# Kernel tuning notes

Hardware: AMD Instinct MI355X
Metric: run time of the kernel (lower is better)

Reference implementation:

```python
import jax, jax.numpy as jnp
import numpy as np

EMBED = 1024
HEADS = 16
HEAD_DIM = EMBED // HEADS
B, S = 2, 2048


def setup_inputs() -> dict:
    key = jax.random.key(0)
    ks = jax.random.split(key, 11)
    sc = 1.0 / np.sqrt(EMBED)
    return {
        "query": jax.random.normal(ks[0], (B, S, EMBED), jnp.float32),
        "key_in": jax.random.normal(ks[1], (B, S, EMBED), jnp.float32),
        "value": jax.random.normal(ks[2], (B, S, EMBED), jnp.float32),
        "Wq": jax.random.normal(ks[3], (EMBED, EMBED), jnp.float32) * sc,
        "bq": jnp.zeros((EMBED,), jnp.float32),
        "Wk": jax.random.normal(ks[4], (EMBED, EMBED), jnp.float32) * sc,
        "bk": jnp.zeros((EMBED,), jnp.float32),
        "Wv": jax.random.normal(ks[5], (EMBED, EMBED), jnp.float32) * sc,
        "bv": jnp.zeros((EMBED,), jnp.float32),
        "Wo": jax.random.normal(ks[6], (EMBED, EMBED), jnp.float32) * sc,
        "bo": jnp.zeros((EMBED,), jnp.float32),
    }


def reference(query, key_in, value, Wq, bq, Wk, bk, Wv, bv, Wo, bo):
    b = query.shape[0]
    # projections -> [B, H, S, Dh]
    def split_heads(x):
        return x.reshape(b, -1, HEADS, HEAD_DIM).transpose(0, 2, 1, 3)
    q = split_heads(query @ Wq + bq)
    k = split_heads(key_in @ Wk + bk)
    v = split_heads(value @ Wv + bv)
    scores = jnp.einsum("bhqd,bhkd->bhqk", q, k) / np.sqrt(HEAD_DIM).astype(jnp.float32)
    probs = jax.nn.softmax(scores, axis=-1)  # dropout in eval mode = identity
    ctx = jnp.einsum("bhqk,bhkd->bhqd", probs, v)
    ctx = ctx.transpose(0, 2, 1, 3).reshape(b, -1, EMBED)
    return ctx @ Wo + bo
```

## Files before the change

kernel.cpp:

```cpp
#include <hip/hip_runtime.h>

typedef unsigned short u16;
typedef unsigned int   u32;
typedef float   f32x4   __attribute__((ext_vector_type(4)));
typedef float   f32x16  __attribute__((ext_vector_type(16)));
typedef __bf16  bf16x8  __attribute__((ext_vector_type(8)));
typedef u16     u16x8   __attribute__((ext_vector_type(8)));
typedef u16     u16x4   __attribute__((ext_vector_type(4)));
typedef u32     u32x4   __attribute__((ext_vector_type(4)));

#define EMBED 1024
#define SEQ   2048
#define NH    16
#define HD    64

#define WS_WT  0u
#define WS_X   (8u<<20)
#define WS_QF  (32u<<20)
#define WS_CTX WS_X
#define WS_KF  (40u<<20)
#define WS_VF  (48u<<20)

__device__ __forceinline__ u16 f2bf(float f) {
  unsigned u = __builtin_bit_cast(unsigned, f);
  u += 0x7fffu + ((u >> 16) & 1u);
  return (u16)(u >> 16);
}

__device__ __forceinline__ u32 cvtpk(float lo, float hi) {
  u32 r;
  asm("v_cvt_pk_bf16_f32 %0, %1, %2" : "=v"(r) : "v"(lo), "v"(hi));
  return r;
}

__device__ __forceinline__ void gl16(const void* g, void* l) {
  __builtin_amdgcn_global_load_lds((__attribute__((address_space(1))) void*)g,
                                   (__attribute__((address_space(3))) void*)l,
                                   16, 0, 0);
}

__global__ __launch_bounds__(256) void cvt_kernel(const float* __restrict__ q,
                                                  const float* __restrict__ k,
                                                  const float* __restrict__ v,
                                                  u16* __restrict__ X) {
  const float* src = blockIdx.z == 0 ? q : blockIdx.z == 1 ? k : v;
  u16* dst = X + (size_t)blockIdx.z * 4194304u;
  size_t i = ((size_t)blockIdx.x * 256 + threadIdx.x) * 8;
  f32x4 a = *(const f32x4*)(src + i);
  f32x4 b = *(const f32x4*)(src + i + 4);
  u16x8 o;
#pragma unroll
  for (int j = 0; j < 4; ++j) { o[j] = f2bf(a[j]); o[4 + j] = f2bf(b[j]); }
  *(u16x8*)(dst + i) = o;
}

__global__ __launch_bounds__(256) void wtrans_kernel(const float* __restrict__ Wq,
                                                     const float* __restrict__ Wk,
                                                     const float* __restrict__ Wv,
                                                     const float* __restrict__ Wo,
                                                     u16* __restrict__ T) {
  const float* W = blockIdx.z == 0 ? Wq : blockIdx.z == 1 ? Wk : blockIdx.z == 2 ? Wv : Wo;
  u16* t = T + (size_t)blockIdx.z * 1048576u;
  __shared__ float sm[32][33];
  const int x = threadIdx.x, y = threadIdx.y;
  const int n0 = blockIdx.x * 32, k0 = blockIdx.y * 32;
#pragma unroll
  for (int i = 0; i < 4; ++i) sm[y + 8 * i][x] = W[(size_t)(k0 + y + 8 * i) * EMBED + n0 + x];
  __syncthreads();
#pragma unroll
  for (int i = 0; i < 4; ++i) t[(size_t)(n0 + y + 8 * i) * EMBED + k0 + x] = f2bf(sm[x][y + 8 * i]);
}

template <int MODE>
__global__ __launch_bounds__(256) void gemm128(char* __restrict__ ws,
                                               const float* __restrict__ bias0,
                                               const float* __restrict__ bias1,
                                               const float* __restrict__ bias2,
                                               float* __restrict__ out) {
  const int z = (MODE == 0) ? blockIdx.z : 0;
  const u16* A  = (MODE == 0) ? (const u16*)(ws + WS_X) + (size_t)z * 4194304u
                              : (const u16*)(ws + WS_CTX);
  const u16* Bt = (const u16*)(ws + WS_WT) + (size_t)((MODE == 0) ? z : 3) * 1048576u;
  const float* bias = (MODE == 0) ? (z == 0 ? bias0 : z == 1 ? bias1 : bias2) : bias0;

  __shared__ u16 lA[128 * 32];
  __shared__ u16 lB[128 * 32];

  const int tid = threadIdx.x, l = tid & 63, w = tid >> 6, g = l >> 4, li = l & 15;

  const int id = blockIdx.y * 8 + blockIdx.x;
  const int swz = (id & 7) * 32 + (id >> 3);
  const int m0 = (swz >> 3) * 128, n0 = (swz & 7) * 128;

  const int wr = (w >> 1) * 64, wc = (w & 1) * 64;
  const int schunk = l & 3;

  f32x4 acc[4][4] = {};

  for (int kt = 0; kt < 32; ++kt) {
    const int k0 = kt * 32;
#pragma unroll
    for (int c = 0; c < 2; ++c) {
      const int ci = w * 2 + c;
      const int row = ci * 16 + (l >> 2);
      const int kk = (schunk ^ (row & 3)) * 8;
      gl16(A + (size_t)(m0 + row) * 1024 + k0 + kk, &lA[ci * 512 + l * 8]);
    }
#pragma unroll
    for (int c = 0; c < 2; ++c) {
      const int ci = w * 2 + c;
      const int row = ci * 16 + (l >> 2);
      const int kk = (schunk ^ (row & 3)) * 8;
      gl16(Bt + (size_t)(n0 + row) * 1024 + k0 + kk, &lB[ci * 512 + l * 8]);
    }
    __syncthreads();

    bf16x8 af[4], bfr[4];
#pragma unroll
    for (int mf = 0; mf < 4; ++mf) {
      const int r = wr + mf * 16 + li;
      af[mf] = __builtin_bit_cast(bf16x8, *(const u16x8*)&lA[r * 32 + (g ^ (r & 3)) * 8]);
    }
#pragma unroll
    for (int nf = 0; nf < 4; ++nf) {
      const int r = wc + nf * 16 + li;
      bfr[nf] = __builtin_bit_cast(bf16x8, *(const u16x8*)&lB[r * 32 + (g ^ (r & 3)) * 8]);
    }
#pragma unroll
    for (int mf = 0; mf < 4; ++mf)
#pragma unroll
      for (int nf = 0; nf < 4; ++nf)
        acc[mf][nf] = __builtin_amdgcn_mfma_f32_16x16x32_bf16(af[mf], bfr[nf], acc[mf][nf], 0, 0, 0);
    __syncthreads();
  }

  u16* Qf = (u16*)(ws + WS_QF);
  u16* Kf = (u16*)(ws + WS_KF);
  u16* Vf = (u16*)(ws + WS_VF);
#pragma unroll
  for (int mf = 0; mf < 4; ++mf)
#pragma unroll
    for (int nf = 0; nf < 4; ++nf)
#pragma unroll
      for (int r4 = 0; r4 < 4; ++r4) {
        const int row = m0 + wr + mf * 16 + g * 4 + r4;
        const int col = n0 + wc + nf * 16 + li;
        float v = acc[mf][nf][r4] + bias[col];
        if (MODE == 1) {
          out[(size_t)row * 1024 + col] = v;
        } else {
          const int bb = row >> 11, s = row & 2047, hh = col >> 6, d = col & 63;
          const size_t fb = (size_t)(bb * 16 + hh) * 131072u;
          const size_t kfo = fb + (s >> 6) * 4096 + ((s >> 5) & 1) * 2048 + (d >> 4) * 512 +
                             ((d >> 3) & 1) * 256 + (s & 31) * 8 + (d & 7);
          if (z == 0) {
            Qf[kfo] = f2bf(v * 0.1803368801f);
          } else if (z == 1) {
            Kf[kfo] = f2bf(v);
          } else {
            const int k16 = s & 15;
            const int ks = (k16 & 3) | ((k16 & 4) << 1) | ((k16 & 8) >> 1);
            Vf[fb + (s >> 6) * 4096 + (d >> 5) * 2048 + ((s >> 5) & 1) * 1024 +
               ((s >> 4) & 1) * 512 + (ks >> 3) * 256 + (d & 31) * 8 + (ks & 7)] = f2bf(v);
          }
        }
      }
}

__global__ __launch_bounds__(64) void attn_kernel(char* __restrict__ ws) {
  const u16* QF = (const u16*)(ws + WS_QF);
  const u16* KF = (const u16*)(ws + WS_KF);
  const u16* VF = (const u16*)(ws + WS_VF);
  u16* ctx = (u16*)(ws + WS_CTX);

  const int l = threadIdx.x, l31 = l & 31, hi = l >> 5;

  const int id = blockIdx.y * 64 + blockIdx.x;
  const int sw = (id & 7) * 256 + (id >> 3);
  const int bh = sw >> 6, qt = sw & 63;

  const u16* Qp = QF + (size_t)bh * 131072u;
  const u16* Kp = KF + (size_t)bh * 131072u;
  const u16* Vp = VF + (size_t)bh * 131072u;
  const int q = qt * 32 + l31;

  bf16x8 qf[4];
#pragma unroll
  for (int kk = 0; kk < 4; ++kk)
    qf[kk] = __builtin_bit_cast(bf16x8, *(const u16x8*)(Qp + (qt * 4 + kk) * 512 + l * 8));

  f32x16 o0 = {}, o1 = {};
  float m = -1e30f, ls = 0.f;

  u16x8 ka[8], kb[8];
#pragma unroll
  for (int g = 0; g < 2; ++g)
#pragma unroll
    for (int kk = 0; kk < 4; ++kk)
      ka[g * 4 + kk] = *(const u16x8*)(Kp + (g * 4 + kk) * 512 + l * 8);

#define ATTN_BODY(KC, KN, T)                                                             \
  {                                                                                      \
    const int tn = ((T) + 1) & 31;                                                       \
    _Pragma("unroll")                                                                    \
    for (int g = 0; g < 2; ++g)                                                          \
      _Pragma("unroll")                                                                  \
      for (int kk = 0; kk < 4; ++kk)                                                     \
        KN[g * 4 + kk] = *(const u16x8*)(Kp + tn * 4096 + (g * 4 + kk) * 512 + l * 8);   \
    u16x8 vf[2][2][2];    \
    _Pragma("unroll")                                                                    \
    for (int g = 0; g < 2; ++g)                                                          \
      _Pragma("unroll")                                                                  \
      for (int dt = 0; dt < 2; ++dt)                                                     \
        _Pragma("unroll")                                                                \
        for (int kk = 0; kk < 2; ++kk)                                                   \
          vf[g][dt][kk] = *(const u16x8*)(Vp + (T) * 4096 +                              \
                                          (dt * 4 + g * 2 + kk) * 512 + l * 8);          \
    f32x16 s0 = {}, s1 = {};                                                             \
    __builtin_amdgcn_s_setprio(1);                                                       \
    _Pragma("unroll")                                                                    \
    for (int kk = 0; kk < 4; ++kk)                                                       \
      s0 = __builtin_amdgcn_mfma_f32_32x32x16_bf16(                                      \
          __builtin_bit_cast(bf16x8, KC[kk]), qf[kk], s0, 0, 0, 0);                      \
    _Pragma("unroll")                                                                    \
    for (int kk = 0; kk < 4; ++kk)                                                       \
      s1 = __builtin_amdgcn_mfma_f32_32x32x16_bf16(                                      \
          __builtin_bit_cast(bf16x8, KC[4 + kk]), qf[kk], s1, 0, 0, 0);                  \
    __builtin_amdgcn_s_setprio(0);                                                       \
    float pm[4] = {-1e30f, -1e30f, -1e30f, -1e30f};                                      \
    _Pragma("unroll")                                                                    \
    for (int r = 0; r < 16; ++r) {                                                       \
      pm[r & 3] = fmaxf(pm[r & 3], s0[r]);                                               \
      pm[r & 3] = fmaxf(pm[r & 3], s1[r]);                                               \
    }                                                                                    \
    float pmax = fmaxf(fmaxf(pm[0], pm[1]), fmaxf(pm[2], pm[3]));                        \
    pmax = fmaxf(pmax, __shfl_xor(pmax, 32));                                            \
    if (__any(pmax > m + 8.0f)) {                                                        \
      const float mn = fmaxf(m, pmax);                                                   \
      const float esc = __builtin_amdgcn_exp2f(m - mn);                                  \
      m = mn;                                                                            \
      ls *= esc;                                                                         \
      _Pragma("unroll")                                                                  \
      for (int r = 0; r < 16; ++r) { o0[r] *= esc; o1[r] *= esc; }                       \
    }                                                                                    \
    float p0[16], p1[16], sr[4] = {0.f, 0.f, 0.f, 0.f};                                  \
    _Pragma("unroll")                                                                    \
    for (int r = 0; r < 16; ++r) {                                                       \
      p0[r] = __builtin_amdgcn_exp2f(s0[r] - m);                                         \
      p1[r] = __builtin_amdgcn_exp2f(s1[r] - m);                                         \
      sr[r & 3] += p0[r] + p1[r];                                                        \
    }                                                                                    \
    float rs = (sr[0] + sr[1]) + (sr[2] + sr[3]);                                        \
    rs += __shfl_xor(rs, 32);                                                            \
    ls += rs;                                                                            \
    u32 pw[16];                                                                          \
    _Pragma("unroll")                                                                    \
    for (int t2 = 0; t2 < 8; ++t2) {                                                     \
      pw[t2] = cvtpk(p0[2 * t2], p0[2 * t2 + 1]);                                        \
      pw[8 + t2] = cvtpk(p1[2 * t2], p1[2 * t2 + 1]);                                    \
    }                                                                                    \
    __builtin_amdgcn_s_setprio(1);                                                       \
    _Pragma("unroll")                                                                    \
    for (int g = 0; g < 2; ++g)                                                          \
      _Pragma("unroll")                                                                  \
      for (int kk = 0; kk < 2; ++kk) {                                                   \
        u32x4 wv = {pw[g * 8 + kk * 4 + 0], pw[g * 8 + kk * 4 + 1],                      \
                    pw[g * 8 + kk * 4 + 2], pw[g * 8 + kk * 4 + 3]};                     \
        bf16x8 pf = __builtin_bit_cast(bf16x8, wv);                                      \
        o0 = __builtin_amdgcn_mfma_f32_32x32x16_bf16(                                    \
            __builtin_bit_cast(bf16x8, vf[g][0][kk]), pf, o0, 0, 0, 0);                  \
        o1 = __builtin_amdgcn_mfma_f32_32x32x16_bf16(                                    \
            __builtin_bit_cast(bf16x8, vf[g][1][kk]), pf, o1, 0, 0, 0);                  \
      }                                                                                  \
    __builtin_amdgcn_s_setprio(0);                                                       \
  }

  for (int tt = 0; tt < 16; ++tt) {
    ATTN_BODY(ka, kb, 2 * tt);
    ATTN_BODY(kb, ka, 2 * tt + 1);
  }
#undef ATTN_BODY

  const int bb = bh >> 4, hh = bh & 15;
  const float rl = 1.0f / ls;
  u16* cp = ctx + ((size_t)bb * SEQ + q) * EMBED + hh * 64;
#pragma unroll
  for (int rr = 0; rr < 4; ++rr) {
    u16x4 ov0, ov1;
#pragma unroll
    for (int j = 0; j < 4; ++j) {
      ov0[j] = f2bf(o0[rr * 4 + j] * rl);
      ov1[j] = f2bf(o1[rr * 4 + j] * rl);
    }
    *(u16x4*)(cp + rr * 8 + hi * 4) = ov0;
    *(u16x4*)(cp + 32 + rr * 8 + hi * 4) = ov1;
  }
}

extern "C" void kernel_launch(void* const* d_in, const int* in_sizes, int n_in,
                              void* d_out, int out_size, void* d_ws, size_t ws_size,
                              hipStream_t stream) {
  const float* q   = (const float*)d_in[0];
  const float* kin = (const float*)d_in[1];
  const float* val = (const float*)d_in[2];
  const float* Wq  = (const float*)d_in[3];
  const float* bq  = (const float*)d_in[4];
  const float* Wk  = (const float*)d_in[5];
  const float* bk  = (const float*)d_in[6];
  const float* Wv  = (const float*)d_in[7];
  const float* bv  = (const float*)d_in[8];
  const float* Wo  = (const float*)d_in[9];
  const float* bo  = (const float*)d_in[10];
  char* ws = (char*)d_ws;
  float* out = (float*)d_out;

  cvt_kernel<<<dim3(2048, 1, 3), 256, 0, stream>>>(q, kin, val, (u16*)(ws + WS_X));
  wtrans_kernel<<<dim3(32, 32, 4), dim3(32, 8), 0, stream>>>(Wq, Wk, Wv, Wo, (u16*)(ws + WS_WT));
  gemm128<0><<<dim3(8, 32, 3), 256, 0, stream>>>(ws, bq, bk, bv, nullptr);
  attn_kernel<<<dim3(64, 32), 64, 0, stream>>>(ws);
  gemm128<1><<<dim3(8, 32, 1), 256, 0, stream>>>(ws, bo, nullptr, nullptr, out);
}
```

Baseline: 136.9 us.

## Software-pipeline QK^T MFMA one tile ahead of softmax and PV

The attention loop now computes the S=QK^T scores for tile T+1 while doing softmax and the PV product for tile T. K is prefetched two tiles ahead, and the first score tile is computed before the loop. The goal is to overlap the matrix-core work with the exp and max ALU work inside one wave. The cost is extra live accumulator registers (two more f32x16), which can lower occupancy or cause spills. The wrap-around also does one redundant score computation at the end.

Result: no change. 138.6 us (+1.2%).

```diff
diff --git a/kernel.cpp b/kernel.cpp
--- a/kernel.cpp
+++ b/kernel.cpp
@@ -196,12 +196,24 @@
 #pragma unroll
   for (int g = 0; g < 2; ++g)
 #pragma unroll
-    for (int kk = 0; kk < 4; ++kk)
+    for (int kk = 0; kk < 4; ++kk) {
       ka[g * 4 + kk] = *(const u16x8*)(Kp + (g * 4 + kk) * 512 + l * 8);
-
-#define ATTN_BODY(KC, KN, T)                                                             \
+      kb[g * 4 + kk] = *(const u16x8*)(Kp + 4096 + (g * 4 + kk) * 512 + l * 8);
+    }
+
+  f32x16 sa0 = {}, sa1 = {}, sb0 = {}, sb1 = {};
+#pragma unroll
+  for (int kk = 0; kk < 4; ++kk)
+    sa0 = __builtin_amdgcn_mfma_f32_32x32x16_bf16(
+        __builtin_bit_cast(bf16x8, ka[kk]), qf[kk], sa0, 0, 0, 0);
+#pragma unroll
+  for (int kk = 0; kk < 4; ++kk)
+    sa1 = __builtin_amdgcn_mfma_f32_32x32x16_bf16(
+        __builtin_bit_cast(bf16x8, ka[4 + kk]), qf[kk], sa1, 0, 0, 0);
+
+#define ATTN_BODY(KC, KN, SC0, SC1, SN0, SN1, T)                                         \
   {                                                                                      \
-    const int tn = ((T) + 1) & 31;                                                       \
+    const int tn = ((T) + 2) & 31;                                                       \
     _Pragma("unroll")                                                                    \
     for (int g = 0; g < 2; ++g)                                                          \
       _Pragma("unroll")                                                                  \
@@ -216,22 +228,23 @@
         for (int kk = 0; kk < 2; ++kk)                                                   \
           vf[g][dt][kk] = *(const u16x8*)(Vp + (T) * 4096 +                              \
                                           (dt * 4 + g * 2 + kk) * 512 + l * 8);          \
-    f32x16 s0 = {}, s1 = {};                                                             \
+    SN0 = (f32x16){};                                                                    \
+    SN1 = (f32x16){};                                                                    \
     __builtin_amdgcn_s_setprio(1);                                                       \
     _Pragma("unroll")                                                                    \
     for (int kk = 0; kk < 4; ++kk)                                                       \
-      s0 = __builtin_amdgcn_mfma_f32_32x32x16_bf16(                                      \
-          __builtin_bit_cast(bf16x8, KC[kk]), qf[kk], s0, 0, 0, 0);                      \
+      SN0 = __builtin_amdgcn_mfma_f32_32x32x16_bf16(                                     \
+          __builtin_bit_cast(bf16x8, KC[kk]), qf[kk], SN0, 0, 0, 0);                     \
     _Pragma("unroll")                                                                    \
     for (int kk = 0; kk < 4; ++kk)                                                       \
-      s1 = __builtin_amdgcn_mfma_f32_32x32x16_bf16(                                      \
-          __builtin_bit_cast(bf16x8, KC[4 + kk]), qf[kk], s1, 0, 0, 0);                  \
+      SN1 = __builtin_amdgcn_mfma_f32_32x32x16_bf16(                                     \
+          __builtin_bit_cast(bf16x8, KC[4 + kk]), qf[kk], SN1, 0, 0, 0);                 \
     __builtin_amdgcn_s_setprio(0);                                                       \
     float pm[4] = {-1e30f, -1e30f, -1e30f, -1e30f};                                      \
     _Pragma("unroll")                                                                    \
     for (int r = 0; r < 16; ++r) {                                                       \
-      pm[r & 3] = fmaxf(pm[r & 3], s0[r]);                                               \
-      pm[r & 3] = fmaxf(pm[r & 3], s1[r]);                                               \
+      pm[r & 3] = fmaxf(pm[r & 3], SC0[r]);                                              \
+      pm[r & 3] = fmaxf(pm[r & 3], SC1[r]);                                              \
     }                                                                                    \
     float pmax = fmaxf(fmaxf(pm[0], pm[1]), fmaxf(pm[2], pm[3]));                        \
     pmax = fmaxf(pmax, __shfl_xor(pmax, 32));                                            \
@@ -246,8 +259,8 @@
     float p0[16], p1[16], sr[4] = {0.f, 0.f, 0.f, 0.f};                                  \
     _Pragma("unroll")                                                                    \
     for (int r = 0; r < 16; ++r) {                                                       \
-      p0[r] = __builtin_amdgcn_exp2f(s0[r] - m);                                         \
-      p1[r] = __builtin_amdgcn_exp2f(s1[r] - m);                                         \
+      p0[r] = __builtin_amdgcn_exp2f(SC0[r] - m);                                        \
+      p1[r] = __builtin_amdgcn_exp2f(SC1[r] - m);                                        \
       sr[r & 3] += p0[r] + p1[r];                                                        \
     }                                                                                    \
     float rs = (sr[0] + sr[1]) + (sr[2] + sr[3]);                                        \
@@ -276,8 +289,8 @@
   }
 
   for (int tt = 0; tt < 16; ++tt) {
-    ATTN_BODY(ka, kb, 2 * tt);
-    ATTN_BODY(kb, ka, 2 * tt + 1);
+    ATTN_BODY(kb, ka, sa0, sa1, sb0, sb1, 2 * tt);
+    ATTN_BODY(ka, kb, sb0, sb1, sa0, sa1, 2 * tt + 1);
   }
 #undef ATTN_BODY
 
```
